# Kernel tuning notes

Hardware: AMD Instinct MI355X
Metric: run time of the kernel (lower is better)

## Reference

```python
import jax, jax.numpy as jnp
import numpy as np

T, B, N, D, H = 128, 64, 24, 256, 8
F = D // H  # 32


def setup_inputs() -> dict:
    key = jax.random.key(0)
    ks = jax.random.split(key, 7)
    s = 1.0 / np.sqrt(D)  # torch nn.Linear default init range
    inputs = jax.random.normal(ks[0], (T, B, N * D), dtype=jnp.float32)
    Wk = jax.random.uniform(ks[1], (H, F, D), minval=-s, maxval=s, dtype=jnp.float32)
    bk = jax.random.uniform(ks[2], (H, F), minval=-s, maxval=s, dtype=jnp.float32)
    Wv = jax.random.uniform(ks[3], (H, F, D), minval=-s, maxval=s, dtype=jnp.float32)
    bv = jax.random.uniform(ks[4], (H, F), minval=-s, maxval=s, dtype=jnp.float32)
    Wq = jax.random.uniform(ks[5], (H, N, F, D), minval=-s, maxval=s, dtype=jnp.float32)
    bq = jax.random.uniform(ks[6], (H, N, F), minval=-s, maxval=s, dtype=jnp.float32)
    return {"inputs": inputs, "Wk": Wk, "bk": bk, "Wv": Wv, "bv": bv, "Wq": Wq, "bq": bq}


def reference(inputs, Wk, bk, Wv, bv, Wq, bq):
    # inputs: (T, B, N*D) -> (T, B, N, D)
    x = inputs.reshape(T, B, N, D)
    # shared K/V per head: (T, B, H, N, F)
    k = jnp.einsum('tbnd,hfd->tbhnf', x, Wk) + bk[:, None, :]
    v = jnp.einsum('tbnd,hfd->tbhnf', x, Wv) + bv[:, None, :]
    # per-joint Q: joint n uses its own (F, D) weight -> (T, B, H, N, F)
    q = jnp.einsum('tbnd,hnfd->tbhnf', x, Wq) + bq
    # attention over joints, scaled by sqrt(F)
    scores = jnp.einsum('tbhnf,tbhmf->tbhnm', q, k) / jnp.sqrt(jnp.float32(F))
    attn = jax.nn.softmax(scores, axis=-1)
    out = jnp.einsum('tbhnm,tbhmf->tbhnf', attn, v)
    # concat heads along feature dim per joint, then flatten joints: (T, B, N*H*F)
    out = out.transpose(0, 1, 3, 2, 4).reshape(T, B, N * H * F)
    # dropout is identity in eval mode
    return out
```

## Files before the change

### kernel.cpp

```cpp
#include <hip/hip_runtime.h>
#include <hip/hip_bf16.h>
#include <cstdio>

#define TB  8192
#define N_  24
#define D_  256
#define H_  8
#define F_  32
#define ND  6144
#define HNF 6144

typedef unsigned short u16;
typedef __attribute__((ext_vector_type(8))) _Float16 f16x8;
typedef __attribute__((ext_vector_type(8))) short bf16x8;
typedef __attribute__((ext_vector_type(4))) float f32x4;

__device__ __forceinline__ u16 f2b(float f) {
    unsigned int u = __float_as_uint(f);
    return (u16)((u + 0x7FFFu + ((u >> 16) & 1u)) >> 16);
}
__device__ __forceinline__ float b2f(u16 s) {
    return __uint_as_float(((unsigned int)s) << 16);
}
__device__ __forceinline__ u16 f2h(float f) {
    _Float16 h = (_Float16)f;
    u16 u; __builtin_memcpy(&u, &h, 2); return u;
}

__device__ __forceinline__ void gl_lds16(const void* g, void* l) {
    __builtin_amdgcn_global_load_lds(
        (const __attribute__((address_space(1))) unsigned int*)g,
        (__attribute__((address_space(3))) unsigned int*)l, 16, 0, 0);
}

__global__ __launch_bounds__(256) void prep_weights(
    const float* __restrict__ Wk, const float* __restrict__ Wv,
    const float* __restrict__ Wq, u16* __restrict__ Bp)
{
    const int idx = blockIdx.x * 256 + threadIdx.x;
    if (idx >= 24 * 8 * 48 * 64) return;
    const int fr = idx & 15;
    const int fq = (idx >> 4) & 3;
    const int g  = (idx >> 6) % 48;
    const int kt = (idx / (64 * 48)) % 8;
    const int n  = idx / (64 * 48 * 8);
    const int col = g * 16 + fr;
    const int d0  = kt * 32 + fq * 8;
    const int c   = col & 255;
    const float* src;
    if (col < 256)      src = Wk + (size_t)c * 256 + d0;
    else if (col < 512) src = Wv + (size_t)c * 256 + d0;
    else {
        const int h = c >> 5, f = c & 31;
        src = Wq + ((size_t)(h * 24 + n) * 32 + f) * 256 + d0;
    }
    __align__(16) u16 out[8];
    #pragma unroll
    for (int j = 0; j < 8; ++j) out[j] = f2h(src[j]);
    *reinterpret_cast<uint4*>(Bp + (size_t)idx * 8) =
        *reinterpret_cast<const uint4*>(out);
}

__global__ __launch_bounds__(256) void prep_bias(
    const float* __restrict__ bk, const float* __restrict__ bv,
    const float* __restrict__ bq, float* __restrict__ biasp)
{
    const int idx = blockIdx.x * 256 + threadIdx.x;
    if (idx >= 24 * 768) return;
    const int col = idx % 768, n = idx / 768;
    const int c = col & 255;
    float v;
    if (col < 256)      v = bk[c];
    else if (col < 512) v = bv[c];
    else { const int h = c >> 5, f = c & 31; v = bq[(h * 24 + n) * 32 + f]; }
    biasp[n * 768 + col] = v;
}

__global__ __launch_bounds__(512, 4) void proj_mfma(
    const float* __restrict__ x,
    const u16* __restrict__ Bp,
    const float* __restrict__ biasp,
    u16* __restrict__ kb, u16* __restrict__ vb, u16* __restrict__ qb)
{
    const int b    = blockIdx.x;
    const int xcd  = b & 7;
    const int t    = b >> 3;
    const int gi   = t % 9;
    const int mblk = t / 9;
    const int grp  = xcd * 9 + gi;
    const int n    = grp / 3;
    const int ct   = grp % 3;
    const int tb0  = mblk * 128;
    const int tid  = threadIdx.x;
    const int w    = tid >> 6;
    const int lane = tid & 63;
    const int wm   = w >> 2;
    const int wn   = w & 3;
    const int fr   = lane & 15, fq = lane >> 4;

    __shared__ __align__(16) char smem[49152];
    char* const Ab = smem;
    char* const Bb = smem + 16384;

    const int arow = tid >> 2;
    const int ac   = tid & 3;
    const float* xsrc = x + (size_t)(tb0 + arow) * ND + n * 256 + ac * 8;
    const int awbyte = arow * 64 + ((ac ^ ((arow >> 1) & 3)) << 4);

    const size_t bbase = (size_t)(n * 8 * 48 + ct * 16 + w * 2) * 1024 + lane * 16;

    f32x4 acc[4][4];
    #pragma unroll
    for (int m = 0; m < 4; ++m)
        #pragma unroll
        for (int j = 0; j < 4; ++j) acc[m][j] = (f32x4){0.f, 0.f, 0.f, 0.f};

    float4 axr[3][2];

    gl_lds16((const char*)Bp + bbase,        Bb + (w * 2) * 1024);
    gl_lds16((const char*)Bp + bbase + 1024, Bb + (w * 2 + 1) * 1024);
    axr[0][0] = *reinterpret_cast<const float4*>(xsrc);
    axr[0][1] = *reinterpret_cast<const float4*>(xsrc + 4);
    axr[1][0] = *reinterpret_cast<const float4*>(xsrc + 32);
    axr[1][1] = *reinterpret_cast<const float4*>(xsrc + 36);
    axr[2][0] = *reinterpret_cast<const float4*>(xsrc + 64);
    axr[2][1] = *reinterpret_cast<const float4*>(xsrc + 68);
    {
        ushort4 hv, hv2;
        hv.x  = f2h(axr[0][0].x); hv.y  = f2h(axr[0][0].y);
        hv.z  = f2h(axr[0][0].z); hv.w  = f2h(axr[0][0].w);
        hv2.x = f2h(axr[0][1].x); hv2.y = f2h(axr[0][1].y);
        hv2.z = f2h(axr[0][1].z); hv2.w = f2h(axr[0][1].w);
        *reinterpret_cast<ushort4*>(Ab + awbyte)     = hv;
        *reinterpret_cast<ushort4*>(Ab + awbyte + 8) = hv2;
    }
    asm volatile("s_waitcnt lgkmcnt(0)" ::: "memory");
    __builtin_amdgcn_s_barrier();
    asm volatile("" ::: "memory");

    #pragma unroll
    for (int kt = 0; kt < 8; ++kt) {
        const int c = kt & 1, o = c ^ 1;

        if (kt < 7) {
            const size_t bs = bbase + (size_t)(kt + 1) * 49152;
            gl_lds16((const char*)Bp + bs,        Bb + o * 16384 + (w * 2) * 1024);
            gl_lds16((const char*)Bp + bs + 1024, Bb + o * 16384 + (w * 2 + 1) * 1024);
        }

        f16x8 bfr[4], afr[4];
        #pragma unroll
        for (int j = 0; j < 4; ++j)
            bfr[j] = *reinterpret_cast<const f16x8*>(
                Bb + c * 16384 + (wn * 4 + j) * 1024 + lane * 16);
        #pragma unroll
        for (int m = 0; m < 4; ++m) {
            const int row = wm * 64 + m * 16 + fr;
            afr[m] = *reinterpret_cast<const f16x8*>(
                Ab + c * 8192 + row * 64 + ((fq ^ ((fr >> 1) & 3)) << 4));
        }
        __builtin_amdgcn_s_setprio(1);
        #pragma unroll
        for (int j = 0; j < 4; ++j)
            #pragma unroll
            for (int m = 0; m < 4; ++m)
                acc[m][j] = __builtin_amdgcn_mfma_f32_16x16x32_f16(
                    afr[m], bfr[j], acc[m][j], 0, 0, 0);
        __builtin_amdgcn_s_setprio(0);

        if (kt < 7) {
            {
                const float4 lo = axr[(kt + 1) % 3][0];
                const float4 hi = axr[(kt + 1) % 3][1];
                ushort4 hv, hv2;
                hv.x  = f2h(lo.x); hv.y  = f2h(lo.y); hv.z  = f2h(lo.z); hv.w  = f2h(lo.w);
                hv2.x = f2h(hi.x); hv2.y = f2h(hi.y); hv2.z = f2h(hi.z); hv2.w = f2h(hi.w);
                *reinterpret_cast<ushort4*>(Ab + o * 8192 + awbyte)     = hv;
                *reinterpret_cast<ushort4*>(Ab + o * 8192 + awbyte + 8) = hv2;
            }
            if (kt < 5) {
                axr[kt % 3][0] = *reinterpret_cast<const float4*>(xsrc + (kt + 3) * 32);
                axr[kt % 3][1] = *reinterpret_cast<const float4*>(xsrc + (kt + 3) * 32 + 4);
            }
            asm volatile("s_waitcnt lgkmcnt(0)" ::: "memory");
            if (kt < 5) { asm volatile("s_waitcnt vmcnt(2)" ::: "memory"); }
            else        { asm volatile("s_waitcnt vmcnt(0)" ::: "memory"); }
            __builtin_amdgcn_s_barrier();
            asm volatile("" ::: "memory");
        }
    }
    __syncthreads();

    u16* dst = (ct == 0) ? kb : (ct == 1) ? vb : qb;
    #pragma unroll
    for (int p = 0; p < 2; ++p) {
        if (wm == p) {
            #pragma unroll
            for (int j = 0; j < 4; ++j) {
                const int colL = wn * 64 + j * 16 + fr;
                const float bs = biasp[n * 768 + ct * 256 + colL];
                #pragma unroll
                for (int m = 0; m < 4; ++m)
                    #pragma unroll
                    for (int r = 0; r < 4; ++r) {
                        const int rowL = m * 16 + fq * 4 + r;
                        const int byte = (rowL * 512 + colL * 2) ^ ((rowL & 7) << 4);
                        *reinterpret_cast<u16*>(smem + byte) = f2b(acc[m][j][r] + bs);
                    }
            }
        }
        __syncthreads();
        #pragma unroll
        for (int it = 0; it < 4; ++it) {
            const int id  = it * 512 + tid;
            const int row = id >> 5;
            const int cch = id & 31;
            const uint4 v = *reinterpret_cast<const uint4*>(
                smem + ((row * 512 + cch * 16) ^ ((row & 7) << 4)));
            *reinterpret_cast<uint4*>(
                &dst[(size_t)(tb0 + p * 64 + row) * HNF + n * 256 + cch * 8]) = v;
        }
        __syncthreads();
    }
}

__device__ __forceinline__ int swz(int row, int chunk) {
    return row * 32 + (((chunk ^ ((row >> 1) ^ (row >> 3))) & 3) << 3);
}

__global__ __launch_bounds__(256) void attn_mfma(
    const u16* __restrict__ kb,
    const u16* __restrict__ vb,
    const u16* __restrict__ qb,
    float* __restrict__ out)
{
    const int tid  = threadIdx.x;
    const int wid  = tid >> 6;
    const int lane = tid & 63;
    const int fr   = lane & 15;
    const int fq   = lane >> 4;
    const size_t tb = (size_t)blockIdx.x * 4 + wid;

    __shared__ __align__(16) u16 lds[4][2048];
    u16* Pw = lds[wid];
    u16* Vt = lds[wid] + 1024;

    #pragma unroll
    for (int i = 0; i < 4; ++i)
        reinterpret_cast<uint4*>(lds[wid])[lane + i * 64] = (uint4){0, 0, 0, 0};

    const u16* qt = qb + tb * HNF;
    const u16* kt = kb + tb * HNF;
    const u16* vt = vb + tb * HNF;
    float* outp = out + tb * ND;

    const float scale = 0.17677669529663687f;
    const bool colok = fr < 8;

    for (int h = 0; h < H_; ++h) {
        const u16* qh = qt + h * 32;
        const u16* kh = kt + h * 32;
        const u16* vh = vt + h * 32;

        bf16x8 qa[2], ka[2];
        #pragma unroll
        for (int t = 0; t < 2; ++t) {
            int rq = t * 16 + fr; rq = rq < 24 ? rq : 23;
            qa[t] = *reinterpret_cast<const bf16x8*>(qh + rq * 256 + fq * 8);
            ka[t] = *reinterpret_cast<const bf16x8*>(kh + rq * 256 + fq * 8);
        }

        {
            const int m = lane >> 2, q = lane & 3;
            const uint4 vv = *reinterpret_cast<const uint4*>(vh + m * 256 + q * 8);
            #pragma unroll
            for (int j = 0; j < 8; ++j) {
                const int f = q * 8 + j;
                Vt[swz(f, m >> 3) + (m & 7)] = reinterpret_cast<const u16*>(&vv)[j];
            }
            if (lane < 32) {
                const int m2 = 16 + (lane >> 2), q2 = lane & 3;
                const uint4 v2 = *reinterpret_cast<const uint4*>(vh + m2 * 256 + q2 * 8);
                #pragma unroll
                for (int j = 0; j < 8; ++j) {
                    const int f = q2 * 8 + j;
                    Vt[swz(f, m2 >> 3) + (m2 & 7)] = reinterpret_cast<const u16*>(&v2)[j];
                }
            }
        }

        f32x4 S[2][2];
        #pragma unroll
        for (int a = 0; a < 2; ++a)
            #pragma unroll
            for (int bb = 0; bb < 2; ++bb)
                S[a][bb] = __builtin_amdgcn_mfma_f32_16x16x32_bf16(
                    qa[a], ka[bb], (f32x4){0.f, 0.f, 0.f, 0.f}, 0, 0, 0);

        float inv[2][4];
        #pragma unroll
        for (int t = 0; t < 2; ++t) {
            float e0[4], e1[4];
            #pragma unroll
            for (int r = 0; r < 4; ++r) {
                const float a = S[t][0][r] * scale;
                const float bbv = colok ? S[t][1][r] * scale : -1e30f;
                float mx = fmaxf(a, bbv);
                #pragma unroll
                for (int off = 1; off < 16; off <<= 1)
                    mx = fmaxf(mx, __shfl_xor(mx, off));
                e0[r] = __expf(a - mx);
                e1[r] = colok ? __expf(bbv - mx) : 0.f;
                float sm = e0[r] + e1[r];
                #pragma unroll
                for (int off = 1; off < 16; off <<= 1)
                    sm += __shfl_xor(sm, off);
                inv[t][r] = 1.f / sm;
            }
            #pragma unroll
            for (int r = 0; r < 4; ++r) {
                const int row = t * 16 + fq * 4 + r;
                if (row < 24) {
                    Pw[swz(row, fr >> 3) + (fr & 7)] = f2b(e0[r]);
                    if (colok) {
                        const int c1 = 16 + fr;
                        Pw[swz(row, c1 >> 3) + (c1 & 7)] = f2b(e1[r]);
                    }
                }
            }
        }

        bf16x8 pa[2], vbf[2];
        #pragma unroll
        for (int t = 0; t < 2; ++t)
            pa[t] = *reinterpret_cast<const bf16x8*>(&Pw[swz(t * 16 + fr, fq)]);
        #pragma unroll
        for (int t = 0; t < 2; ++t)
            vbf[t] = *reinterpret_cast<const bf16x8*>(&Vt[swz(t * 16 + fr, fq)]);

        f32x4 O[2][2];
        #pragma unroll
        for (int a = 0; a < 2; ++a)
            #pragma unroll
            for (int bb = 0; bb < 2; ++bb)
                O[a][bb] = __builtin_amdgcn_mfma_f32_16x16x32_bf16(
                    pa[a], vbf[bb], (f32x4){0.f, 0.f, 0.f, 0.f}, 0, 0, 0);

        #pragma unroll
        for (int a = 0; a < 2; ++a)
            #pragma unroll
            for (int r = 0; r < 4; ++r) {
                const int row = a * 16 + fq * 4 + r;
                if (row < 24) {
                    outp[row * D_ + h * F_ + fr]      = O[a][0][r] * inv[a][r];
                    outp[row * D_ + h * F_ + 16 + fr] = O[a][1][r] * inv[a][r];
                }
            }
    }
}

extern "C" void kernel_launch(void* const* d_in, const int* in_sizes, int n_in,
                              void* d_out, int out_size, void* d_ws, size_t ws_size,
                              hipStream_t stream) {
    const float* x  = (const float*)d_in[0];
    const float* Wk = (const float*)d_in[1];
    const float* bk = (const float*)d_in[2];
    const float* Wv = (const float*)d_in[3];
    const float* bv = (const float*)d_in[4];
    const float* Wq = (const float*)d_in[5];
    const float* bq = (const float*)d_in[6];
    float* out = (float*)d_out;

    const size_t qkv_elems = (size_t)TB * HNF;
    const size_t need = qkv_elems * 2ull * 3ull;
    if (ws_size < need) fprintf(stderr, "ws too small: %zu < %zu\n", ws_size, need);
    u16* kbuf = (u16*)d_ws;
    u16* vbuf = kbuf + qkv_elems;
    u16* qbuf = vbuf + qkv_elems;

    u16*   Bp    = (u16*)d_out;
    float* biasp = (float*)((char*)d_out + (size_t)24 * 8 * 48 * 512 * 2);

    prep_weights<<<2304, 256, 0, stream>>>(Wk, Wv, Wq, Bp);
    prep_bias<<<(24 * 768 + 255) / 256, 256, 0, stream>>>(bk, bv, bq, biasp);
    proj_mfma<<<4608, 512, 0, stream>>>(x, Bp, biasp, kbuf, vbuf, qbuf);
    attn_mfma<<<TB / 4, 256, 0, stream>>>(kbuf, vbuf, qbuf, out);
}
```

Before: 290.5 us.

## Stream fp32 activations directly to LDS and merge weight/bias prep kernels

The projection kernel now loads raw fp32 activation tiles straight into LDS with async global-to-LDS copies in a triple-buffered, XOR-swizzled layout, and converts to fp16 at fragment-read time. The register staging, in-register conversion and LDS store path are dropped, and the A loads are pipelined two k-steps ahead. This raises LDS use from 48KB to 80KB per block, which may reduce occupancy below the requested 4 blocks, and does the conversion redundantly in each wave. The two prep kernels are also merged into one launch to save a launch.

```diff
diff --git a/kernel.cpp b/kernel.cpp
--- a/kernel.cpp
+++ b/kernel.cpp
@@ -33,47 +33,45 @@
         (__attribute__((address_space(3))) unsigned int*)l, 16, 0, 0);
 }
 
-__global__ __launch_bounds__(256) void prep_weights(
+__global__ __launch_bounds__(256) void prep_all(
     const float* __restrict__ Wk, const float* __restrict__ Wv,
-    const float* __restrict__ Wq, u16* __restrict__ Bp)
+    const float* __restrict__ Wq,
+    const float* __restrict__ bk, const float* __restrict__ bv,
+    const float* __restrict__ bq,
+    u16* __restrict__ Bp, float* __restrict__ biasp)
 {
     const int idx = blockIdx.x * 256 + threadIdx.x;
-    if (idx >= 24 * 8 * 48 * 64) return;
-    const int fr = idx & 15;
-    const int fq = (idx >> 4) & 3;
-    const int g  = (idx >> 6) % 48;
-    const int kt = (idx / (64 * 48)) % 8;
-    const int n  = idx / (64 * 48 * 8);
-    const int col = g * 16 + fr;
-    const int d0  = kt * 32 + fq * 8;
-    const int c   = col & 255;
-    const float* src;
-    if (col < 256)      src = Wk + (size_t)c * 256 + d0;
-    else if (col < 512) src = Wv + (size_t)c * 256 + d0;
-    else {
-        const int h = c >> 5, f = c & 31;
-        src = Wq + ((size_t)(h * 24 + n) * 32 + f) * 256 + d0;
+    if (idx < 24 * 8 * 48 * 64) {
+        const int fr = idx & 15;
+        const int fq = (idx >> 4) & 3;
+        const int g  = (idx >> 6) % 48;
+        const int kt = (idx / (64 * 48)) % 8;
+        const int n  = idx / (64 * 48 * 8);
+        const int col = g * 16 + fr;
+        const int d0  = kt * 32 + fq * 8;
+        const int c   = col & 255;
+        const float* src;
+        if (col < 256)      src = Wk + (size_t)c * 256 + d0;
+        else if (col < 512) src = Wv + (size_t)c * 256 + d0;
+        else {
+            const int h = c >> 5, f = c & 31;
+            src = Wq + ((size_t)(h * 24 + n) * 32 + f) * 256 + d0;
+        }
+        __align__(16) u16 out[8];
+        #pragma unroll
+        for (int j = 0; j < 8; ++j) out[j] = f2h(src[j]);
+        *reinterpret_cast<uint4*>(Bp + (size_t)idx * 8) =
+            *reinterpret_cast<const uint4*>(out);
+    } else if (idx < 24 * 8 * 48 * 64 + 24 * 768) {
+        const int bi  = idx - 24 * 8 * 48 * 64;
+        const int col = bi % 768, n = bi / 768;
+        const int c = col & 255;
+        float v;
+        if (col < 256)      v = bk[c];
+        else if (col < 512) v = bv[c];
+        else { const int h = c >> 5, f = c & 31; v = bq[(h * 24 + n) * 32 + f]; }
+        biasp[n * 768 + col] = v;
     }
-    __align__(16) u16 out[8];
-    #pragma unroll
-    for (int j = 0; j < 8; ++j) out[j] = f2h(src[j]);
-    *reinterpret_cast<uint4*>(Bp + (size_t)idx * 8) =
-        *reinterpret_cast<const uint4*>(out);
-}
-
-__global__ __launch_bounds__(256) void prep_bias(
-    const float* __restrict__ bk, const float* __restrict__ bv,
-    const float* __restrict__ bq, float* __restrict__ biasp)
-{
-    const int idx = blockIdx.x * 256 + threadIdx.x;
-    if (idx >= 24 * 768) return;
-    const int col = idx % 768, n = idx / 768;
-    const int c = col & 255;
-    float v;
-    if (col < 256)      v = bk[c];
-    else if (col < 512) v = bv[c];
-    else { const int h = c >> 5, f = c & 31; v = bq[(h * 24 + n) * 32 + f]; }
-    biasp[n * 768 + col] = v;
 }
 
 __global__ __launch_bounds__(512, 4) void proj_mfma(
@@ -98,14 +96,14 @@
     const int wn   = w & 3;
     const int fr   = lane & 15, fq = lane >> 4;
 
-    __shared__ __align__(16) char smem[49152];
+    __shared__ __align__(16) char smem[81920];
     char* const Ab = smem;
-    char* const Bb = smem + 16384;
-
-    const int arow = tid >> 2;
-    const int ac   = tid & 3;
-    const float* xsrc = x + (size_t)(tb0 + arow) * ND + n * 256 + ac * 8;
-    const int awbyte = arow * 64 + ((ac ^ ((arow >> 1) & 3)) << 4);
+    char* const Bb = smem + 49152;
+
+    const int arow8 = lane >> 3;
+    const int clog  = (lane & 7) ^ arow8;
+    const char* asrc = (const char*)x +
+        (size_t)(tb0 + w * 16 + arow8) * (ND * 4) + n * 1024 + clog * 16;
 
     const size_t bbase = (size_t)(n * 8 * 48 + ct * 16 + w * 2) * 1024 + lane * 16;
 
@@ -115,50 +113,57 @@
         #pragma unroll
         for (int j = 0; j < 4; ++j) acc[m][j] = (f32x4){0.f, 0.f, 0.f, 0.f};
 
-    float4 axr[3][2];
-
+    #pragma unroll
+    for (int q = 0; q < 2; ++q)
+        gl_lds16(asrc + q * (8 * ND * 4), Ab + (w * 2 + q) * 1024);
     gl_lds16((const char*)Bp + bbase,        Bb + (w * 2) * 1024);
     gl_lds16((const char*)Bp + bbase + 1024, Bb + (w * 2 + 1) * 1024);
-    axr[0][0] = *reinterpret_cast<const float4*>(xsrc);
-    axr[0][1] = *reinterpret_cast<const float4*>(xsrc + 4);
-    axr[1][0] = *reinterpret_cast<const float4*>(xsrc + 32);
-    axr[1][1] = *reinterpret_cast<const float4*>(xsrc + 36);
-    axr[2][0] = *reinterpret_cast<const float4*>(xsrc + 64);
-    axr[2][1] = *reinterpret_cast<const float4*>(xsrc + 68);
-    {
-        ushort4 hv, hv2;
-        hv.x  = f2h(axr[0][0].x); hv.y  = f2h(axr[0][0].y);
-        hv.z  = f2h(axr[0][0].z); hv.w  = f2h(axr[0][0].w);
-        hv2.x = f2h(axr[0][1].x); hv2.y = f2h(axr[0][1].y);
-        hv2.z = f2h(axr[0][1].z); hv2.w = f2h(axr[0][1].w);
-        *reinterpret_cast<ushort4*>(Ab + awbyte)     = hv;
-        *reinterpret_cast<ushort4*>(Ab + awbyte + 8) = hv2;
-    }
-    asm volatile("s_waitcnt lgkmcnt(0)" ::: "memory");
+    #pragma unroll
+    for (int q = 0; q < 2; ++q)
+        gl_lds16(asrc + q * (8 * ND * 4) + 128, Ab + 16384 + (w * 2 + q) * 1024);
+    asm volatile("s_waitcnt vmcnt(2)" ::: "memory");
     __builtin_amdgcn_s_barrier();
     asm volatile("" ::: "memory");
 
     #pragma unroll
     for (int kt = 0; kt < 8; ++kt) {
-        const int c = kt & 1, o = c ^ 1;
+        const int ab  = kt % 3;
+        const int bbf = kt & 1;
 
         if (kt < 7) {
             const size_t bs = bbase + (size_t)(kt + 1) * 49152;
-            gl_lds16((const char*)Bp + bs,        Bb + o * 16384 + (w * 2) * 1024);
-            gl_lds16((const char*)Bp + bs + 1024, Bb + o * 16384 + (w * 2 + 1) * 1024);
+            gl_lds16((const char*)Bp + bs,        Bb + (bbf ^ 1) * 16384 + (w * 2) * 1024);
+            gl_lds16((const char*)Bp + bs + 1024, Bb + (bbf ^ 1) * 16384 + (w * 2 + 1) * 1024);
+        }
+        if (kt < 6) {
+            #pragma unroll
+            for (int q = 0; q < 2; ++q)
+                gl_lds16(asrc + q * (8 * ND * 4) + (kt + 2) * 128,
+                         Ab + ((kt + 2) % 3) * 16384 + (w * 2 + q) * 1024);
         }
 
         f16x8 bfr[4], afr[4];
         #pragma unroll
         for (int j = 0; j < 4; ++j)
             bfr[j] = *reinterpret_cast<const f16x8*>(
-                Bb + c * 16384 + (wn * 4 + j) * 1024 + lane * 16);
+                Bb + bbf * 16384 + (wn * 4 + j) * 1024 + lane * 16);
         #pragma unroll
         for (int m = 0; m < 4; ++m) {
             const int row = wm * 64 + m * 16 + fr;
-            afr[m] = *reinterpret_cast<const f16x8*>(
-                Ab + c * 8192 + row * 64 + ((fq ^ ((fr >> 1) & 3)) << 4));
-        }
+            const int c0  = (2 * fq) ^ (fr & 7);
+            const f32x4 lo = *reinterpret_cast<const f32x4*>(
+                Ab + ab * 16384 + row * 128 + c0 * 16);
+            const f32x4 hi = *reinterpret_cast<const f32x4*>(
+                Ab + ab * 16384 + row * 128 + (c0 ^ 1) * 16);
+            f16x8 af;
+            #pragma unroll
+            for (int e = 0; e < 4; ++e) {
+                af[e]     = (_Float16)lo[e];
+                af[4 + e] = (_Float16)hi[e];
+            }
+            afr[m] = af;
+        }
+
         __builtin_amdgcn_s_setprio(1);
         #pragma unroll
         for (int j = 0; j < 4; ++j)
@@ -169,21 +174,7 @@
         __builtin_amdgcn_s_setprio(0);
 
         if (kt < 7) {
-            {
-                const float4 lo = axr[(kt + 1) % 3][0];
-                const float4 hi = axr[(kt + 1) % 3][1];
-                ushort4 hv, hv2;
-                hv.x  = f2h(lo.x); hv.y  = f2h(lo.y); hv.z  = f2h(lo.z); hv.w  = f2h(lo.w);
-                hv2.x = f2h(hi.x); hv2.y = f2h(hi.y); hv2.z = f2h(hi.z); hv2.w = f2h(hi.w);
-                *reinterpret_cast<ushort4*>(Ab + o * 8192 + awbyte)     = hv;
-                *reinterpret_cast<ushort4*>(Ab + o * 8192 + awbyte + 8) = hv2;
-            }
-            if (kt < 5) {
-                axr[kt % 3][0] = *reinterpret_cast<const float4*>(xsrc + (kt + 3) * 32);
-                axr[kt % 3][1] = *reinterpret_cast<const float4*>(xsrc + (kt + 3) * 32 + 4);
-            }
-            asm volatile("s_waitcnt lgkmcnt(0)" ::: "memory");
-            if (kt < 5) { asm volatile("s_waitcnt vmcnt(2)" ::: "memory"); }
+            if (kt < 6) { asm volatile("s_waitcnt vmcnt(2)" ::: "memory"); }
             else        { asm volatile("s_waitcnt vmcnt(0)" ::: "memory"); }
             __builtin_amdgcn_s_barrier();
             asm volatile("" ::: "memory");
@@ -381,8 +372,7 @@
     u16*   Bp    = (u16*)d_out;
     float* biasp = (float*)((char*)d_out + (size_t)24 * 8 * 48 * 512 * 2);
 
-    prep_weights<<<2304, 256, 0, stream>>>(Wk, Wv, Wq, Bp);
-    prep_bias<<<(24 * 768 + 255) / 256, 256, 0, stream>>>(bk, bv, bq, biasp);
+    prep_all<<<2376, 256, 0, stream>>>(Wk, Wv, Wq, bk, bv, bq, Bp, biasp);
     proj_mfma<<<4608, 512, 0, stream>>>(x, Bp, biasp, kbuf, vbuf, qbuf);
     attn_mfma<<<TB / 4, 256, 0, stream>>>(kbuf, vbuf, qbuf, out);
 }
```

New measurement: 286.4 us. Within noise of the previous version (-1.4%).

## Keep full weight slice resident in LDS and process two M-blocks per workgroup

Applied to the files above, without the earlier changes.

The projection kernel now loads all 8 K-tiles of its weight slice into a 128 KB LDS buffer once, then reuses it across two consecutive 128-row M-blocks. The grid is halved and the x loads are pipelined across both blocks. This cuts repeated weight traffic and per-block B staging. The epilogue is split into four 32-row passes through a smaller staging area. The two weight-prep kernels are also fused into one launch. The cost is a much larger LDS footprint (about 144 KB), which lowers occupancy (launch bounds go from 4 to 2) and may reduce latency hiding.

```diff
diff --git a/kernel.cpp b/kernel.cpp
--- a/kernel.cpp
+++ b/kernel.cpp
@@ -33,50 +33,48 @@
         (__attribute__((address_space(3))) unsigned int*)l, 16, 0, 0);
 }
 
-__global__ __launch_bounds__(256) void prep_weights(
+__global__ __launch_bounds__(256) void prep_all(
     const float* __restrict__ Wk, const float* __restrict__ Wv,
-    const float* __restrict__ Wq, u16* __restrict__ Bp)
+    const float* __restrict__ Wq,
+    const float* __restrict__ bk, const float* __restrict__ bv,
+    const float* __restrict__ bq,
+    u16* __restrict__ Bp, float* __restrict__ biasp)
 {
     const int idx = blockIdx.x * 256 + threadIdx.x;
-    if (idx >= 24 * 8 * 48 * 64) return;
-    const int fr = idx & 15;
-    const int fq = (idx >> 4) & 3;
-    const int g  = (idx >> 6) % 48;
-    const int kt = (idx / (64 * 48)) % 8;
-    const int n  = idx / (64 * 48 * 8);
-    const int col = g * 16 + fr;
-    const int d0  = kt * 32 + fq * 8;
-    const int c   = col & 255;
-    const float* src;
-    if (col < 256)      src = Wk + (size_t)c * 256 + d0;
-    else if (col < 512) src = Wv + (size_t)c * 256 + d0;
-    else {
-        const int h = c >> 5, f = c & 31;
-        src = Wq + ((size_t)(h * 24 + n) * 32 + f) * 256 + d0;
+    if (idx < 24 * 8 * 48 * 64) {
+        const int fr = idx & 15;
+        const int fq = (idx >> 4) & 3;
+        const int g  = (idx >> 6) % 48;
+        const int kt = (idx / (64 * 48)) % 8;
+        const int n  = idx / (64 * 48 * 8);
+        const int col = g * 16 + fr;
+        const int d0  = kt * 32 + fq * 8;
+        const int c   = col & 255;
+        const float* src;
+        if (col < 256)      src = Wk + (size_t)c * 256 + d0;
+        else if (col < 512) src = Wv + (size_t)c * 256 + d0;
+        else {
+            const int h = c >> 5, f = c & 31;
+            src = Wq + ((size_t)(h * 24 + n) * 32 + f) * 256 + d0;
+        }
+        __align__(16) u16 out[8];
+        #pragma unroll
+        for (int j = 0; j < 8; ++j) out[j] = f2h(src[j]);
+        *reinterpret_cast<uint4*>(Bp + (size_t)idx * 8) =
+            *reinterpret_cast<const uint4*>(out);
+    } else if (idx < 24 * 8 * 48 * 64 + 24 * 768) {
+        const int bi  = idx - 24 * 8 * 48 * 64;
+        const int col = bi % 768, n = bi / 768;
+        const int c = col & 255;
+        float v;
+        if (col < 256)      v = bk[c];
+        else if (col < 512) v = bv[c];
+        else { const int h = c >> 5, f = c & 31; v = bq[(h * 24 + n) * 32 + f]; }
+        biasp[n * 768 + col] = v;
     }
-    __align__(16) u16 out[8];
-    #pragma unroll
-    for (int j = 0; j < 8; ++j) out[j] = f2h(src[j]);
-    *reinterpret_cast<uint4*>(Bp + (size_t)idx * 8) =
-        *reinterpret_cast<const uint4*>(out);
-}
-
-__global__ __launch_bounds__(256) void prep_bias(
-    const float* __restrict__ bk, const float* __restrict__ bv,
-    const float* __restrict__ bq, float* __restrict__ biasp)
-{
-    const int idx = blockIdx.x * 256 + threadIdx.x;
-    if (idx >= 24 * 768) return;
-    const int col = idx % 768, n = idx / 768;
-    const int c = col & 255;
-    float v;
-    if (col < 256)      v = bk[c];
-    else if (col < 512) v = bv[c];
-    else { const int h = c >> 5, f = c & 31; v = bq[(h * 24 + n) * 32 + f]; }
-    biasp[n * 768 + col] = v;
-}
-
-__global__ __launch_bounds__(512, 4) void proj_mfma(
+}
+
+__global__ __launch_bounds__(512, 2) void proj_mfma(
     const float* __restrict__ x,
     const u16* __restrict__ Bp,
     const float* __restrict__ biasp,
@@ -86,11 +84,10 @@
     const int xcd  = b & 7;
     const int t    = b >> 3;
     const int gi   = t % 9;
-    const int mblk = t / 9;
+    const int mch  = t / 9;
     const int grp  = xcd * 9 + gi;
     const int n    = grp / 3;
     const int ct   = grp % 3;
-    const int tb0  = mblk * 128;
     const int tid  = threadIdx.x;
     const int w    = tid >> 6;
     const int lane = tid & 63;
@@ -98,33 +95,33 @@
     const int wn   = w & 3;
     const int fr   = lane & 15, fq = lane >> 4;
 
-    __shared__ __align__(16) char smem[49152];
-    char* const Ab = smem;
-    char* const Bb = smem + 16384;
+    __shared__ __align__(16) char smem[147456];
+    char* const Bs = smem;
+    char* const Ab = smem + 131072;
+    char* const Eb = smem + 131072;
 
     const int arow = tid >> 2;
     const int ac   = tid & 3;
-    const float* xsrc = x + (size_t)(tb0 + arow) * ND + n * 256 + ac * 8;
+    const float* xsrc0 = x + (size_t)(mch * 256 + arow) * ND + n * 256 + ac * 8;
     const int awbyte = arow * 64 + ((ac ^ ((arow >> 1) & 3)) << 4);
 
-    const size_t bbase = (size_t)(n * 8 * 48 + ct * 16 + w * 2) * 1024 + lane * 16;
-
-    f32x4 acc[4][4];
+    u16* dst = (ct == 0) ? kb : (ct == 1) ? vb : qb;
+
+    float4 axr[3][2];
+
+    axr[0][0] = *reinterpret_cast<const float4*>(xsrc0);
+    axr[0][1] = *reinterpret_cast<const float4*>(xsrc0 + 4);
     #pragma unroll
-    for (int m = 0; m < 4; ++m)
-        #pragma unroll
-        for (int j = 0; j < 4; ++j) acc[m][j] = (f32x4){0.f, 0.f, 0.f, 0.f};
-
-    float4 axr[3][2];
-
-    gl_lds16((const char*)Bp + bbase,        Bb + (w * 2) * 1024);
-    gl_lds16((const char*)Bp + bbase + 1024, Bb + (w * 2 + 1) * 1024);
-    axr[0][0] = *reinterpret_cast<const float4*>(xsrc);
-    axr[0][1] = *reinterpret_cast<const float4*>(xsrc + 4);
-    axr[1][0] = *reinterpret_cast<const float4*>(xsrc + 32);
-    axr[1][1] = *reinterpret_cast<const float4*>(xsrc + 36);
-    axr[2][0] = *reinterpret_cast<const float4*>(xsrc + 64);
-    axr[2][1] = *reinterpret_cast<const float4*>(xsrc + 68);
+    for (int kt = 0; kt < 8; ++kt) {
+        const char* bsrc = (const char*)Bp +
+            (size_t)((n * 8 + kt) * 48 + ct * 16 + w * 2) * 1024 + (size_t)lane * 16;
+        gl_lds16(bsrc,        Bs + kt * 16384 + (w * 2) * 1024);
+        gl_lds16(bsrc + 1024, Bs + kt * 16384 + (w * 2 + 1) * 1024);
+    }
+    axr[1][0] = *reinterpret_cast<const float4*>(xsrc0 + 32);
+    axr[1][1] = *reinterpret_cast<const float4*>(xsrc0 + 36);
+    axr[2][0] = *reinterpret_cast<const float4*>(xsrc0 + 64);
+    axr[2][1] = *reinterpret_cast<const float4*>(xsrc0 + 68);
     {
         ushort4 hv, hv2;
         hv.x  = f2h(axr[0][0].x); hv.y  = f2h(axr[0][0].y);
@@ -135,92 +132,123 @@
         *reinterpret_cast<ushort4*>(Ab + awbyte + 8) = hv2;
     }
     asm volatile("s_waitcnt lgkmcnt(0)" ::: "memory");
+    asm volatile("s_waitcnt vmcnt(4)" ::: "memory");
     __builtin_amdgcn_s_barrier();
     asm volatile("" ::: "memory");
 
     #pragma unroll
-    for (int kt = 0; kt < 8; ++kt) {
-        const int c = kt & 1, o = c ^ 1;
-
-        if (kt < 7) {
-            const size_t bs = bbase + (size_t)(kt + 1) * 49152;
-            gl_lds16((const char*)Bp + bs,        Bb + o * 16384 + (w * 2) * 1024);
-            gl_lds16((const char*)Bp + bs + 1024, Bb + o * 16384 + (w * 2 + 1) * 1024);
-        }
-
-        f16x8 bfr[4], afr[4];
-        #pragma unroll
-        for (int j = 0; j < 4; ++j)
-            bfr[j] = *reinterpret_cast<const f16x8*>(
-                Bb + c * 16384 + (wn * 4 + j) * 1024 + lane * 16);
-        #pragma unroll
-        for (int m = 0; m < 4; ++m) {
-            const int row = wm * 64 + m * 16 + fr;
-            afr[m] = *reinterpret_cast<const f16x8*>(
-                Ab + c * 8192 + row * 64 + ((fq ^ ((fr >> 1) & 3)) << 4));
-        }
-        __builtin_amdgcn_s_setprio(1);
-        #pragma unroll
-        for (int j = 0; j < 4; ++j)
-            #pragma unroll
-            for (int m = 0; m < 4; ++m)
-                acc[m][j] = __builtin_amdgcn_mfma_f32_16x16x32_f16(
-                    afr[m], bfr[j], acc[m][j], 0, 0, 0);
-        __builtin_amdgcn_s_setprio(0);
-
-        if (kt < 7) {
-            {
-                const float4 lo = axr[(kt + 1) % 3][0];
-                const float4 hi = axr[(kt + 1) % 3][1];
-                ushort4 hv, hv2;
-                hv.x  = f2h(lo.x); hv.y  = f2h(lo.y); hv.z  = f2h(lo.z); hv.w  = f2h(lo.w);
-                hv2.x = f2h(hi.x); hv2.y = f2h(hi.y); hv2.z = f2h(hi.z); hv2.w = f2h(hi.w);
-                *reinterpret_cast<ushort4*>(Ab + o * 8192 + awbyte)     = hv;
-                *reinterpret_cast<ushort4*>(Ab + o * 8192 + awbyte + 8) = hv2;
-            }
-            if (kt < 5) {
-                axr[kt % 3][0] = *reinterpret_cast<const float4*>(xsrc + (kt + 3) * 32);
-                axr[kt % 3][1] = *reinterpret_cast<const float4*>(xsrc + (kt + 3) * 32 + 4);
+    for (int mb = 0; mb < 2; ++mb) {
+        f32x4 acc[4][4];
+        #pragma unroll
+        for (int m = 0; m < 4; ++m)
+            #pragma unroll
+            for (int j = 0; j < 4; ++j) acc[m][j] = (f32x4){0.f, 0.f, 0.f, 0.f};
+
+        #pragma unroll
+        for (int kt = 0; kt < 8; ++kt) {
+            const int s = mb * 8 + kt;
+            const int c = kt & 1, o = c ^ 1;
+
+            f16x8 bfr[4], afr[4];
+            #pragma unroll
+            for (int j = 0; j < 4; ++j)
+                bfr[j] = *reinterpret_cast<const f16x8*>(
+                    Bs + kt * 16384 + (wn * 4 + j) * 1024 + lane * 16);
+            #pragma unroll
+            for (int m = 0; m < 4; ++m) {
+                const int row = wm * 64 + m * 16 + fr;
+                afr[m] = *reinterpret_cast<const f16x8*>(
+                    Ab + c * 8192 + row * 64 + ((fq ^ ((fr >> 1) & 3)) << 4));
+            }
+            __builtin_amdgcn_s_setprio(1);
+            #pragma unroll
+            for (int j = 0; j < 4; ++j)
+                #pragma unroll
+                for (int m = 0; m < 4; ++m)
+                    acc[m][j] = __builtin_amdgcn_mfma_f32_16x16x32_f16(
+                        afr[m], bfr[j], acc[m][j], 0, 0, 0);
+            __builtin_amdgcn_s_setprio(0);
+
+            if (kt < 7) {
+                {
+                    const float4 lo = axr[(s + 1) % 3][0];
+                    const float4 hi = axr[(s + 1) % 3][1];
+                    ushort4 hv, hv2;
+                    hv.x  = f2h(lo.x); hv.y  = f2h(lo.y); hv.z  = f2h(lo.z); hv.w  = f2h(lo.w);
+                    hv2.x = f2h(hi.x); hv2.y = f2h(hi.y); hv2.z = f2h(hi.z); hv2.w = f2h(hi.w);
+                    *reinterpret_cast<ushort4*>(Ab + o * 8192 + awbyte)     = hv;
+                    *reinterpret_cast<ushort4*>(Ab + o * 8192 + awbyte + 8) = hv2;
+                }
+                if (s + 3 < 16) {
+                    const int s3 = s + 3;
+                    const float* p = xsrc0 + (size_t)(s3 >> 3) * (128 * ND) + (s3 & 7) * 32;
+                    axr[s3 % 3][0] = *reinterpret_cast<const float4*>(p);
+                    axr[s3 % 3][1] = *reinterpret_cast<const float4*>(p + 4);
+                }
+                asm volatile("s_waitcnt lgkmcnt(0)" ::: "memory");
+                __builtin_amdgcn_s_barrier();
+                asm volatile("" ::: "memory");
+            } else if (mb == 0) {
+                const float* p = xsrc0 + (size_t)(10 >> 3) * (128 * ND) + (10 & 7) * 32;
+                axr[1][0] = *reinterpret_cast<const float4*>(p);
+                axr[1][1] = *reinterpret_cast<const float4*>(p + 4);
+            }
+        }
+
+        asm volatile("s_waitcnt lgkmcnt(0)" ::: "memory");
+        __builtin_amdgcn_s_barrier();
+        asm volatile("" ::: "memory");
+
+        const int tb0 = mch * 256 + mb * 128;
+        #pragma unroll
+        for (int p = 0; p < 4; ++p) {
+            if (wm == (p >> 1)) {
+                #pragma unroll
+                for (int mm = 0; mm < 2; ++mm) {
+                    const int m = (p & 1) * 2 + mm;
+                    #pragma unroll
+                    for (int j = 0; j < 4; ++j) {
+                        const int colL = wn * 64 + j * 16 + fr;
+                        const float bs = biasp[n * 768 + ct * 256 + colL];
+                        #pragma unroll
+                        for (int r = 0; r < 4; ++r) {
+                            const int rowL = mm * 16 + fq * 4 + r;
+                            const int byte = (rowL * 512 + colL * 2) ^ ((rowL & 7) << 4);
+                            *reinterpret_cast<u16*>(Eb + byte) = f2b(acc[m][j][r] + bs);
+                        }
+                    }
+                }
             }
             asm volatile("s_waitcnt lgkmcnt(0)" ::: "memory");
-            if (kt < 5) { asm volatile("s_waitcnt vmcnt(2)" ::: "memory"); }
-            else        { asm volatile("s_waitcnt vmcnt(0)" ::: "memory"); }
             __builtin_amdgcn_s_barrier();
             asm volatile("" ::: "memory");
-        }
-    }
-    __syncthreads();
-
-    u16* dst = (ct == 0) ? kb : (ct == 1) ? vb : qb;
-    #pragma unroll
-    for (int p = 0; p < 2; ++p) {
-        if (wm == p) {
-            #pragma unroll
-            for (int j = 0; j < 4; ++j) {
-                const int colL = wn * 64 + j * 16 + fr;
-                const float bs = biasp[n * 768 + ct * 256 + colL];
-                #pragma unroll
-                for (int m = 0; m < 4; ++m)
-                    #pragma unroll
-                    for (int r = 0; r < 4; ++r) {
-                        const int rowL = m * 16 + fq * 4 + r;
-                        const int byte = (rowL * 512 + colL * 2) ^ ((rowL & 7) << 4);
-                        *reinterpret_cast<u16*>(smem + byte) = f2b(acc[m][j][r] + bs);
-                    }
-            }
-        }
-        __syncthreads();
-        #pragma unroll
-        for (int it = 0; it < 4; ++it) {
-            const int id  = it * 512 + tid;
-            const int row = id >> 5;
-            const int cch = id & 31;
-            const uint4 v = *reinterpret_cast<const uint4*>(
-                smem + ((row * 512 + cch * 16) ^ ((row & 7) << 4)));
-            *reinterpret_cast<uint4*>(
-                &dst[(size_t)(tb0 + p * 64 + row) * HNF + n * 256 + cch * 8]) = v;
-        }
-        __syncthreads();
+            #pragma unroll
+            for (int it = 0; it < 2; ++it) {
+                const int id  = it * 512 + tid;
+                const int row = id >> 5;
+                const int cch = id & 31;
+                const uint4 v = *reinterpret_cast<const uint4*>(
+                    Eb + ((row * 512 + cch * 16) ^ ((row & 7) << 4)));
+                *reinterpret_cast<uint4*>(
+                    &dst[(size_t)(tb0 + p * 32 + row) * HNF + n * 256 + cch * 8]) = v;
+            }
+            asm volatile("s_waitcnt lgkmcnt(0)" ::: "memory");
+            __builtin_amdgcn_s_barrier();
+            asm volatile("" ::: "memory");
+        }
+
+        if (mb == 0) {
+            const float4 lo = axr[8 % 3][0];
+            const float4 hi = axr[8 % 3][1];
+            ushort4 hv, hv2;
+            hv.x  = f2h(lo.x); hv.y  = f2h(lo.y); hv.z  = f2h(lo.z); hv.w  = f2h(lo.w);
+            hv2.x = f2h(hi.x); hv2.y = f2h(hi.y); hv2.z = f2h(hi.z); hv2.w = f2h(hi.w);
+            *reinterpret_cast<ushort4*>(Ab + awbyte)     = hv;
+            *reinterpret_cast<ushort4*>(Ab + awbyte + 8) = hv2;
+            asm volatile("s_waitcnt lgkmcnt(0)" ::: "memory");
+            __builtin_amdgcn_s_barrier();
+            asm volatile("" ::: "memory");
+        }
     }
 }
 
@@ -381,8 +409,7 @@
     u16*   Bp    = (u16*)d_out;
     float* biasp = (float*)((char*)d_out + (size_t)24 * 8 * 48 * 512 * 2);
 
-    prep_weights<<<2304, 256, 0, stream>>>(Wk, Wv, Wq, Bp);
-    prep_bias<<<(24 * 768 + 255) / 256, 256, 0, stream>>>(bk, bv, bq, biasp);
-    proj_mfma<<<4608, 512, 0, stream>>>(x, Bp, biasp, kbuf, vbuf, qbuf);
+    prep_all<<<2376, 256, 0, stream>>>(Wk, Wv, Wq, bk, bv, bq, Bp, biasp);
+    proj_mfma<<<2304, 512, 0, stream>>>(x, Bp, biasp, kbuf, vbuf, qbuf);
     attn_mfma<<<TB / 4, 256, 0, stream>>>(kbuf, vbuf, qbuf, out);
 }
```

Measured after the change: 313.1 us. 7.8% more time.
